# Kernel tuning notes

Hardware: AMD Instinct MI355X
Metric: run time of the kernel (lower is better)

The kernel has to match this reference:

```python
import jax, jax.numpy as jnp
import numpy as np

N, E, H, L = 50000, 1_600_000, 128, 3


def _ln(x, g, b, eps=1e-5):
    m = x.mean(-1, keepdims=True)
    v = x.var(-1, keepdims=True)
    return (x - m) / jnp.sqrt(v + eps) * g + b


def _mlp2(inp, w1, b1, g, be, w2, b2):
    # Linear -> LayerNorm -> SiLU -> (Dropout=identity in eval) -> Linear
    h = inp @ w1 + b1
    h = jax.nn.silu(_ln(h, g, be))
    return h @ w2 + b2


def setup_inputs() -> dict:
    key = jax.random.key(0)
    ks = jax.random.split(key, 16)
    s = 0.05
    inp = {
        'x': jax.random.normal(ks[0], (N, 7), jnp.float32),
        'pos': jax.random.normal(ks[1], (N, 3), jnp.float32),
        'edge_index': jax.random.randint(ks[2], (2, E), 0, N, jnp.int64),
        'enc_w1': jax.random.normal(ks[3], (7, H)) * s,
        'enc_b1': jnp.zeros((H,)),
        'enc_g': jnp.ones((H,)),
        'enc_be': jnp.zeros((H,)),
        'enc_w2': jax.random.normal(ks[4], (H, H)) * s,
        'enc_b2': jnp.zeros((H,)),
        'e_w1': jax.random.normal(ks[5], (L, 2 * H + 5, H)) * s,
        'e_b1': jnp.zeros((L, H)),
        'e_g': jnp.ones((L, H)),
        'e_be': jnp.zeros((L, H)),
        'e_w2': jax.random.normal(ks[6], (L, H, H)) * s,
        'e_b2': jnp.zeros((L, H)),
        'n_w1': jax.random.normal(ks[7], (L, 2 * H, H)) * s,
        'n_b1': jnp.zeros((L, H)),
        'n_g': jnp.ones((L, H)),
        'n_be': jnp.zeros((L, H)),
        'n_w2': jax.random.normal(ks[8], (L, H, H)) * s,
        'n_b2': jnp.zeros((L, H)),
        'ln_g': jnp.ones((L, H)),
        'ln_b': jnp.zeros((L, H)),
        'dec_w1': jax.random.normal(ks[9], (H, H)) * s,
        'dec_b1': jnp.zeros((H,)),
        'dec_w2': jax.random.normal(ks[10], (H, H // 2)) * s,
        'dec_b2': jnp.zeros((H // 2,)),
        'dec_w3': jax.random.normal(ks[11], (H // 2, 6)) * s,
        'dec_b3': jnp.zeros((6,)),
    }
    return inp


def reference(x, pos, edge_index, enc_w1, enc_b1, enc_g, enc_be, enc_w2, enc_b2,
              e_w1, e_b1, e_g, e_be, e_w2, e_b2,
              n_w1, n_b1, n_g, n_be, n_w2, n_b2,
              ln_g, ln_b, dec_w1, dec_b1, dec_w2, dec_b2, dec_w3, dec_b3):
    n_nodes = x.shape[0]
    row, col = edge_index[0], edge_index[1]  # row=source(j), col=target(i)

    # physics edge features: [dist, direction(3), 1/r^2]
    diff = pos[col] - pos[row]                          # (E,3)
    dist = jnp.linalg.norm(diff, axis=-1, keepdims=True) + 1e-8
    edge_attr = jnp.concatenate([dist, diff / dist, 1.0 / (dist ** 2 + 1e-6)], -1)

    h = _mlp2(x, enc_w1, enc_b1, enc_g, enc_be, enc_w2, enc_b2)  # (N,H)

    for l in range(L):
        # message: cat(x_i, x_j, edge_attr) -> edge MLP
        msg_in = jnp.concatenate([h[col], h[row], edge_attr], -1)  # (E,2H+5)
        msg = _mlp2(msg_in, e_w1[l], e_b1[l], e_g[l], e_be[l], e_w2[l], e_b2[l])
        # scatter-add aggregate to targets
        aggr = jax.ops.segment_sum(msg, col, num_segments=n_nodes)  # (N,H)
        # update: cat(x, aggr) -> node MLP, then residual + LayerNorm
        h_new = _mlp2(jnp.concatenate([h, aggr], -1),
                      n_w1[l], n_b1[l], n_g[l], n_be[l], n_w2[l], n_b2[l])
        h = _ln(h + h_new, ln_g[l], ln_b[l])

    d = jax.nn.silu(h @ dec_w1 + dec_b1)
    d = jax.nn.silu(d @ dec_w2 + dec_b2)
    delta = d @ dec_w3 + dec_b3                                  # (N,6)
    return x[:, :6] + delta
```

## Files before the change

kernel.cpp:

```cpp
#include <hip/hip_runtime.h>

typedef unsigned short u16;
typedef unsigned int u32;
typedef __bf16 bf16x8 __attribute__((ext_vector_type(8)));
typedef float f32x4 __attribute__((ext_vector_type(4)));
typedef float f32x2 __attribute__((ext_vector_type(2)));

#define AS_STRIDE 136

__device__ __forceinline__ u16 f2bf1(float f) {
  union { __bf16 h; u16 u; } c; c.h = (__bf16)f; return c.u;
}
__device__ __forceinline__ u32 cvt2bf(float a, float b) {
  union { __bf16 h[2]; u32 u; } c; c.h[0] = (__bf16)a; c.h[1] = (__bf16)b; return c.u;
}
__device__ __forceinline__ float bf2f(u16 u) {
  union { u32 u; float f; } v; v.u = ((u32)u) << 16; return v.f;
}
__device__ __forceinline__ float silu_f(float a) {
  return a * __builtin_amdgcn_rcpf(1.f + __expf(-a));
}
__device__ __forceinline__ float rsq_f(float x) {
  return __builtin_amdgcn_rsqf(x);
}
__device__ __forceinline__ f32x2 unpk2(u32 p) {
  union { u32 u; float f; } a, b;
  a.u = p << 16; b.u = p & 0xffff0000u;
  return (f32x2){a.f, b.f};
}

__global__ void edge_hist(const int* __restrict__ edst, int E, int* __restrict__ cnt) {
  int i = blockIdx.x * blockDim.x + threadIdx.x;
  if (i < E) atomicAdd(&cnt[edst[i]], 1);
}

__global__ __launch_bounds__(1024)
void scan_kernel(const int* __restrict__ cnt, int* __restrict__ cursor, int Nn) {
  __shared__ int part[1024];
  int t = threadIdx.x;
  int per = (Nn + 1023) / 1024;
  int b = t * per;
  int s = 0;
  for (int i = 0; i < per; i++) { int idx = b + i; if (idx < Nn) s += cnt[idx]; }
  part[t] = s;
  __syncthreads();
  for (int d = 1; d < 1024; d <<= 1) {
    int v = (t >= d) ? part[t - d] : 0;
    __syncthreads();
    part[t] += v;
    __syncthreads();
  }
  int excl = (t == 0) ? 0 : part[t - 1];
  for (int i = 0; i < per; i++) {
    int idx = b + i;
    if (idx < Nn) { cursor[idx] = excl; excl += cnt[idx]; }
  }
}

__global__ void edge_scatter(const int* __restrict__ esrc, const int* __restrict__ edst,
                             int E, int* __restrict__ cursor,
                             int* __restrict__ ssrc, int* __restrict__ sdst) {
  int i = blockIdx.x * blockDim.x + threadIdx.x;
  if (i < E) {
    int d = edst[i];
    int p = atomicAdd(&cursor[d], 1);
    ssrc[p] = esrc[i];
    sdst[p] = d;
  }
}

__global__ void prep_weights(const float* __restrict__ e_w1, const float* __restrict__ e_w2,
                             const float* __restrict__ n_w1, const float* __restrict__ n_w2,
                             u16* __restrict__ eW1T, u16* __restrict__ eW2T,
                             u16* __restrict__ nW1T, u16* __restrict__ nW2T) {
  int i = blockIdx.x * blockDim.x + threadIdx.x;
  const int s1 = 3 * 128 * 256;
  const int s2 = 3 * 128 * 128;
  if (i < s1) {
    int l = i / 32768, r = i % 32768, n = r >> 8, k = r & 255;
    eW1T[i] = f2bf1(e_w1[l * 33408 + k * 128 + n]);
  } else if (i < s1 + s2) {
    int j = i - s1; int l = j / 16384, r = j % 16384, n = r >> 7, k = r & 127;
    eW2T[j] = f2bf1(e_w2[l * 16384 + k * 128 + n]);
  } else if (i < s1 + s2 + s1) {
    int j = i - s1 - s2; int l = j / 32768, r = j % 32768, n = r >> 8, k = r & 255;
    nW1T[j] = f2bf1(n_w1[l * 32768 + k * 128 + n]);
  } else if (i < 2 * s1 + 2 * s2) {
    int j = i - 2 * s1 - s2; int l = j / 16384, r = j % 16384, n = r >> 7, k = r & 127;
    nW2T[j] = f2bf1(n_w2[l * 16384 + k * 128 + n]);
  }
}

__global__ void prep_weights2(const float* __restrict__ enc_w1, const float* __restrict__ enc_w2,
                              const float* __restrict__ dec_w1, const float* __restrict__ dec_w2,
                              const float* __restrict__ dec_w3, const float* __restrict__ e_w1,
                              u16* __restrict__ encW1T, u16* __restrict__ encW2T,
                              u16* __restrict__ decW1T, u16* __restrict__ decW2T,
                              u16* __restrict__ decW3T, u16* __restrict__ eW1cT) {
  int i = blockIdx.x * blockDim.x + threadIdx.x;
  if (i < 4096) {
    int n = i >> 5, k = i & 31;
    encW1T[i] = (k < 7) ? f2bf1(enc_w1[k * 128 + n]) : (u16)0;
  } else if (i < 20480) {
    int j = i - 4096; int n = j >> 7, k = j & 127;
    encW2T[j] = f2bf1(enc_w2[k * 128 + n]);
  } else if (i < 36864) {
    int j = i - 20480; int n = j >> 7, k = j & 127;
    decW1T[j] = f2bf1(dec_w1[k * 128 + n]);
  } else if (i < 45056) {
    int j = i - 36864; int n = j >> 7, k = j & 127;
    decW2T[j] = f2bf1(dec_w2[k * 64 + n]);
  } else if (i < 46080) {
    int j = i - 45056; int n = j >> 6, k = j & 63;
    decW3T[j] = (n < 6) ? f2bf1(dec_w3[k * 6 + n]) : (u16)0;
  } else if (i < 58368) {
    int j = i - 46080; int l = j / 4096, r = j % 4096, n = r >> 5, k = r & 31;
    eW1cT[j] = (k < 5) ? f2bf1(e_w1[l * 33408 + (256 + k) * 128 + n]) : (u16)0;
  }
}

__global__ __launch_bounds__(256, 4)
void encoder_mfma(const float* __restrict__ x,
                  const u16* __restrict__ W1T,
                  const float* __restrict__ b1,
                  const float* __restrict__ g, const float* __restrict__ be,
                  const u16* __restrict__ W2T,
                  const float* __restrict__ b2,
                  const u16* __restrict__ eW1T0,
                  const float* __restrict__ eb10,
                  u16* __restrict__ hbf, u16* __restrict__ hd_all,
                  u16* __restrict__ hs_all, int Nn) {
  __shared__ __align__(16) u16 As[64 * 40];
  __shared__ __align__(16) u16 ts[64 * AS_STRIDE];
  const int tid = threadIdx.x;
  const int m0 = blockIdx.x * 64;
  const int w = tid >> 6, lane = tid & 63, quad = lane >> 4, l16 = lane & 15;
  const int c0w = w * 32;

  if (tid < 64) {
    int node = m0 + tid; if (node >= Nn) node = Nn - 1;
    union { u16 us[32]; uint4 v[4]; } pk;
    #pragma unroll
    for (int k = 0; k < 32; k++) pk.us[k] = 0;
    #pragma unroll
    for (int k = 0; k < 7; k++) pk.us[k] = f2bf1(x[node * 7 + k]);
    #pragma unroll
    for (int k = 0; k < 4; k++) *(uint4*)(As + tid * 40 + k * 8) = pk.v[k];
  }
  __syncthreads();

  f32x4 acc[4][2];
  #pragma unroll
  for (int rt = 0; rt < 4; rt++)
    #pragma unroll
    for (int ct = 0; ct < 2; ct++)
      acc[rt][ct] = (f32x4){0.f, 0.f, 0.f, 0.f};
  {
    const int kl = quad * 8;
    bf16x8 af[4];
    #pragma unroll
    for (int rt = 0; rt < 4; rt++)
      af[rt] = *(const bf16x8*)(As + (rt * 16 + l16) * 40 + kl);
    #pragma unroll
    for (int ct = 0; ct < 2; ct++) {
      bf16x8 bfv = *(const bf16x8*)(W1T + (c0w + ct * 16 + l16) * 32 + kl);
      #pragma unroll
      for (int rt = 0; rt < 4; rt++)
        acc[rt][ct] = __builtin_amdgcn_mfma_f32_16x16x32_bf16(af[rt], bfv, acc[rt][ct], 0, 0, 0);
    }
  }
  #pragma unroll
  for (int ct = 0; ct < 2; ct++) {
    int n = c0w + ct * 16 + l16;
    float b1v = b1[n];
    #pragma unroll
    for (int rt = 0; rt < 4; rt++)
      #pragma unroll
      for (int r = 0; r < 4; r++)
        ts[(rt * 16 + quad * 4 + r) * AS_STRIDE + n] = f2bf1(acc[rt][ct][r] + b1v);
  }
  __syncthreads();

  {
    int row = tid >> 2, sub = tid & 3;
    float s = 0.f, sq = 0.f, vals[32];
    #pragma unroll
    for (int i = 0; i < 32; i++) {
      float v = bf2f(ts[row * AS_STRIDE + sub + i * 4]);
      vals[i] = v; s += v; sq += v * v;
    }
    s += __shfl_xor(s, 1); sq += __shfl_xor(sq, 1);
    s += __shfl_xor(s, 2); sq += __shfl_xor(sq, 2);
    float mean = s * (1.f / 128.f);
    float rstd = rsq_f(sq * (1.f / 128.f) - mean * mean + 1e-5f);
    #pragma unroll
    for (int i = 0; i < 32; i++) {
      int c = sub + i * 4;
      float a = (vals[i] - mean) * rstd * g[c] + be[c];
      ts[row * AS_STRIDE + c] = f2bf1(silu_f(a));
    }
  }
  __syncthreads();

  f32x4 acc2[4][2];
  #pragma unroll
  for (int rt = 0; rt < 4; rt++)
    #pragma unroll
    for (int ct = 0; ct < 2; ct++)
      acc2[rt][ct] = (f32x4){0.f, 0.f, 0.f, 0.f};
  #pragma unroll
  for (int kk = 0; kk < 4; kk++) {
    const int kl = kk * 32 + quad * 8;
    bf16x8 af[4];
    #pragma unroll
    for (int rt = 0; rt < 4; rt++)
      af[rt] = *(const bf16x8*)(ts + (rt * 16 + l16) * AS_STRIDE + kl);
    #pragma unroll
    for (int ct = 0; ct < 2; ct++) {
      bf16x8 bfv = *(const bf16x8*)(W2T + (size_t)(c0w + ct * 16 + l16) * 128 + kl);
      #pragma unroll
      for (int rt = 0; rt < 4; rt++)
        acc2[rt][ct] = __builtin_amdgcn_mfma_f32_16x16x32_bf16(af[rt], bfv, acc2[rt][ct], 0, 0, 0);
    }
  }
  __syncthreads();
  #pragma unroll
  for (int ct = 0; ct < 2; ct++) {
    int n = c0w + ct * 16 + l16;
    float b2v = b2[n];
    #pragma unroll
    for (int rt = 0; rt < 4; rt++)
      #pragma unroll
      for (int r = 0; r < 4; r++) {
        int m = rt * 16 + quad * 4 + r;
        int node = m0 + m;
        u16 hb = f2bf1(acc2[rt][ct][r] + b2v);
        ts[m * AS_STRIDE + n] = hb;
        if (node < Nn) hbf[(size_t)node * 128 + n] = hb;
      }
  }
  __syncthreads();

  {
    f32x4 ah[4][2];
    #pragma unroll
    for (int rt = 0; rt < 4; rt++)
      #pragma unroll
      for (int ct = 0; ct < 2; ct++)
        ah[rt][ct] = (f32x4){0.f, 0.f, 0.f, 0.f};
    #pragma unroll
    for (int kk = 0; kk < 4; kk++) {
      const int kl = kk * 32 + quad * 8;
      bf16x8 af[4];
      #pragma unroll
      for (int rt = 0; rt < 4; rt++)
        af[rt] = *(const bf16x8*)(ts + (rt * 16 + l16) * AS_STRIDE + kl);
      #pragma unroll
      for (int ct = 0; ct < 2; ct++) {
        bf16x8 bd = *(const bf16x8*)(eW1T0 + (size_t)(c0w + ct * 16 + l16) * 256 + kl);
        #pragma unroll
        for (int rt = 0; rt < 4; rt++)
          ah[rt][ct] = __builtin_amdgcn_mfma_f32_16x16x32_bf16(af[rt], bd, ah[rt][ct], 0, 0, 0);
      }
    }
    #pragma unroll
    for (int ct = 0; ct < 2; ct++) {
      int n = c0w + ct * 16 + l16;
      float b1v = eb10[n];
      #pragma unroll
      for (int rt = 0; rt < 4; rt++)
        #pragma unroll
        for (int r = 0; r < 4; r++) {
          int node = m0 + rt * 16 + quad * 4 + r;
          if (node < Nn) hd_all[(size_t)node * 128 + n] = f2bf1(ah[rt][ct][r] + b1v);
        }
    }
    #pragma unroll
    for (int rt = 0; rt < 4; rt++)
      #pragma unroll
      for (int ct = 0; ct < 2; ct++)
        ah[rt][ct] = (f32x4){0.f, 0.f, 0.f, 0.f};
    #pragma unroll
    for (int kk = 0; kk < 4; kk++) {
      const int kl = kk * 32 + quad * 8;
      bf16x8 af[4];
      #pragma unroll
      for (int rt = 0; rt < 4; rt++)
        af[rt] = *(const bf16x8*)(ts + (rt * 16 + l16) * AS_STRIDE + kl);
      #pragma unroll
      for (int ct = 0; ct < 2; ct++) {
        bf16x8 bs = *(const bf16x8*)(eW1T0 + (size_t)(c0w + ct * 16 + l16) * 256 + 128 + kl);
        #pragma unroll
        for (int rt = 0; rt < 4; rt++)
          ah[rt][ct] = __builtin_amdgcn_mfma_f32_16x16x32_bf16(af[rt], bs, ah[rt][ct], 0, 0, 0);
      }
    }
    #pragma unroll
    for (int ct = 0; ct < 2; ct++) {
      int n = c0w + ct * 16 + l16;
      #pragma unroll
      for (int rt = 0; rt < 4; rt++)
        #pragma unroll
        for (int r = 0; r < 4; r++) {
          int node = m0 + rt * 16 + quad * 4 + r;
          if (node < Nn) hs_all[(size_t)node * 128 + n] = f2bf1(ah[rt][ct][r]);
        }
    }
  }
}

__global__ __launch_bounds__(256, 4)
void edge_mlp_kernel(const int* __restrict__ ssrc, const int* __restrict__ sdst,
                     const float* __restrict__ pos,
                     const u16* __restrict__ hd_all, const u16* __restrict__ hs_all,
                     const u16* __restrict__ w1cT,
                     const float* __restrict__ g, const float* __restrict__ be,
                     const u16* __restrict__ W2T,
                     const float* __restrict__ b2,
                     float* __restrict__ aggr) {
  __shared__ int s_dst[64];
  __shared__ __align__(16) u16 s_eaA[64 * 40];
  __shared__ __align__(16) u16 s_t[64 * AS_STRIDE];
  __shared__ __align__(16) u16 s_msg[128 * 68];

  const int tid = threadIdx.x;
  const int bid = blockIdx.x;
  const int e0 = ((bid & 7) * (gridDim.x >> 3) + (bid >> 3)) * 64;
  const int w = tid >> 6, lane = tid & 63, quad = lane >> 4, l16 = lane & 15;
  const int c0w = w * 32;
  const int rg = tid >> 4, cg = tid & 15;
  const int c0 = cg * 8;

  int pdst[4], psrc[4];
  #pragma unroll
  for (int rr = 0; rr < 4; rr++) {
    pdst[rr] = sdst[e0 + rg * 4 + rr];
    psrc[rr] = ssrc[e0 + rg * 4 + rr];
  }
  uint4 hd4[4], hs4[4];
  #pragma unroll
  for (int rr = 0; rr < 4; rr++) {
    hd4[rr] = *(const uint4*)(hd_all + (size_t)pdst[rr] * 128 + c0);
    hs4[rr] = *(const uint4*)(hs_all + (size_t)psrc[rr] * 128 + c0);
  }
  asm volatile("" ::: "memory");

  if (tid < 64) {
    int src = ssrc[e0 + tid], dst = sdst[e0 + tid];
    s_dst[tid] = dst;
    float dx = pos[dst * 3 + 0] - pos[src * 3 + 0];
    float dy = pos[dst * 3 + 1] - pos[src * 3 + 1];
    float dz = pos[dst * 3 + 2] - pos[src * 3 + 2];
    float dist = sqrtf(dx * dx + dy * dy + dz * dz) + 1e-8f;
    float inv = __builtin_amdgcn_rcpf(dist);
    union { u16 us[40]; uint4 v[5]; } pk;
    #pragma unroll
    for (int k = 0; k < 40; k++) pk.us[k] = 0;
    pk.us[0] = f2bf1(dist);
    pk.us[1] = f2bf1(dx * inv); pk.us[2] = f2bf1(dy * inv); pk.us[3] = f2bf1(dz * inv);
    pk.us[4] = f2bf1(__builtin_amdgcn_rcpf(dist * dist + 1e-6f));
    #pragma unroll
    for (int k = 0; k < 5; k++) *(uint4*)(s_eaA + tid * 40 + k * 8) = pk.v[k];
  }
  __syncthreads();

  {
    f32x4 ae[4][2];
    #pragma unroll
    for (int rt = 0; rt < 4; rt++)
      #pragma unroll
      for (int ct = 0; ct < 2; ct++)
        ae[rt][ct] = (f32x4){0.f, 0.f, 0.f, 0.f};
    const int kl = quad * 8;
    bf16x8 afe[4];
    #pragma unroll
    for (int rt = 0; rt < 4; rt++)
      afe[rt] = *(const bf16x8*)(s_eaA + (rt * 16 + l16) * 40 + kl);
    #pragma unroll
    for (int ct = 0; ct < 2; ct++) {
      bf16x8 bw = *(const bf16x8*)(w1cT + (c0w + ct * 16 + l16) * 32 + kl);
      #pragma unroll
      for (int rt = 0; rt < 4; rt++)
        ae[rt][ct] = __builtin_amdgcn_mfma_f32_16x16x32_bf16(afe[rt], bw, ae[rt][ct], 0, 0, 0);
    }
    #pragma unroll
    for (int ct = 0; ct < 2; ct++) {
      int n = c0w + ct * 16 + l16;
      #pragma unroll
      for (int rt = 0; rt < 4; rt++)
        #pragma unroll
        for (int r = 0; r < 4; r++)
          s_t[(rt * 16 + quad * 4 + r) * AS_STRIDE + n] = f2bf1(ae[rt][ct][r]);
    }
  }
  __syncthreads();

  {
    f32x2 g2[4], be2[4];
    {
      f32x4 ga = *(const f32x4*)(g + c0), gb = *(const f32x4*)(g + c0 + 4);
      f32x4 ba = *(const f32x4*)(be + c0), bb = *(const f32x4*)(be + c0 + 4);
      g2[0] = (f32x2){ga[0], ga[1]}; g2[1] = (f32x2){ga[2], ga[3]};
      g2[2] = (f32x2){gb[0], gb[1]}; g2[3] = (f32x2){gb[2], gb[3]};
      be2[0] = (f32x2){ba[0], ba[1]}; be2[1] = (f32x2){ba[2], ba[3]};
      be2[2] = (f32x2){bb[0], bb[1]}; be2[3] = (f32x2){bb[2], bb[3]};
    }
    #pragma unroll
    for (int rr = 0; rr < 4; rr++) {
      int m = rg * 4 + rr;
      uint4 te4 = *(const uint4*)(s_t + m * AS_STRIDE + c0);
      u32 hp[4] = {hd4[rr].x, hd4[rr].y, hd4[rr].z, hd4[rr].w};
      u32 sp[4] = {hs4[rr].x, hs4[rr].y, hs4[rr].z, hs4[rr].w};
      u32 tp[4] = {te4.x, te4.y, te4.z, te4.w};
      f32x2 t2[4], sm2 = (f32x2){0.f, 0.f}, sq2 = (f32x2){0.f, 0.f};
      #pragma unroll
      for (int p = 0; p < 4; p++) {
        t2[p] = unpk2(hp[p]) + unpk2(sp[p]) + unpk2(tp[p]);
        sm2 += t2[p];
        sq2 += t2[p] * t2[p];
      }
      float sm = sm2[0] + sm2[1], sq = sq2[0] + sq2[1];
      sm += __shfl_xor(sm, 1);  sq += __shfl_xor(sq, 1);
      sm += __shfl_xor(sm, 2);  sq += __shfl_xor(sq, 2);
      sm += __shfl_xor(sm, 4);  sq += __shfl_xor(sq, 4);
      sm += __shfl_xor(sm, 8);  sq += __shfl_xor(sq, 8);
      float mean = sm * (1.f / 128.f);
      float rstd = rsq_f(sq * (1.f / 128.f) - mean * mean + 1e-5f);
      f32x2 sc = (f32x2){rstd, rstd};
      f32x2 ofs = (f32x2){-mean * rstd, -mean * rstd};
      float o[8];
      #pragma unroll
      for (int p = 0; p < 4; p++) {
        f32x2 a = t2[p] * sc + ofs;
        a = a * g2[p] + be2[p];
        o[2 * p]     = silu_f(a[0]);
        o[2 * p + 1] = silu_f(a[1]);
      }
      uint4 st;
      st.x = cvt2bf(o[0], o[1]); st.y = cvt2bf(o[2], o[3]);
      st.z = cvt2bf(o[4], o[5]); st.w = cvt2bf(o[6], o[7]);
      *(uint4*)(s_t + m * AS_STRIDE + c0) = st;
    }
  }
  __syncthreads();

  f32x4 acc2[4][2];
  #pragma unroll
  for (int rt = 0; rt < 4; rt++)
    #pragma unroll
    for (int ct = 0; ct < 2; ct++)
      acc2[rt][ct] = (f32x4){0.f, 0.f, 0.f, 0.f};

  #pragma unroll
  for (int kk = 0; kk < 4; kk++) {
    const int kl = kk * 32 + quad * 8;
    bf16x8 af[4];
    #pragma unroll
    for (int rt = 0; rt < 4; rt++)
      af[rt] = *(const bf16x8*)(s_t + (rt * 16 + l16) * AS_STRIDE + kl);
    #pragma unroll
    for (int ct = 0; ct < 2; ct++) {
      bf16x8 bfv = *(const bf16x8*)(W2T + (size_t)(c0w + ct * 16 + l16) * 128 + kl);
      #pragma unroll
      for (int rt = 0; rt < 4; rt++)
        acc2[rt][ct] = __builtin_amdgcn_mfma_f32_16x16x32_bf16(af[rt], bfv, acc2[rt][ct], 0, 0, 0);
    }
  }

  #pragma unroll
  for (int ct = 0; ct < 2; ct++) {
    int n = c0w + ct * 16 + l16;
    float b2v = b2[n];
    #pragma unroll
    for (int rt = 0; rt < 4; rt++) {
      int mb = rt * 16 + quad * 4;
      uint2 st;
      st.x = cvt2bf(acc2[rt][ct][0] + b2v, acc2[rt][ct][1] + b2v);
      st.y = cvt2bf(acc2[rt][ct][2] + b2v, acc2[rt][ct][3] + b2v);
      *(uint2*)(s_msg + n * 68 + mb) = st;
    }
  }
  __syncthreads();

  {
    int c = tid & 127, q = tid >> 7;
    int r0 = q * 32;
    const u16* mp = s_msg + c * 68 + r0;
    float run = 0.f; int cur = s_dst[r0];
    #pragma unroll
    for (int i = 0; i < 8; i++) {
      uint2 pr = *(const uint2*)(mp + 4 * i);
      union { u32 u; float f; } va, vb, vc, vd;
      va.u = pr.x << 16; vb.u = pr.x & 0xffff0000u;
      vc.u = pr.y << 16; vd.u = pr.y & 0xffff0000u;
      int rb = r0 + 4 * i;
      int d0 = s_dst[rb], d1 = s_dst[rb + 1], d2 = s_dst[rb + 2], d3 = s_dst[rb + 3];
      if (d0 != cur) { atomicAdd(&aggr[(size_t)cur * 128 + c], run); run = 0.f; cur = d0; }
      run += va.f;
      if (d1 != cur) { atomicAdd(&aggr[(size_t)cur * 128 + c], run); run = 0.f; cur = d1; }
      run += vb.f;
      if (d2 != cur) { atomicAdd(&aggr[(size_t)cur * 128 + c], run); run = 0.f; cur = d2; }
      run += vc.f;
      if (d3 != cur) { atomicAdd(&aggr[(size_t)cur * 128 + c], run); run = 0.f; cur = d3; }
      run += vd.f;
    }
    atomicAdd(&aggr[(size_t)cur * 128 + c], run);
  }
}

__global__ __launch_bounds__(256, 4)
void node_mlp_kernel(u16* __restrict__ hbf, float* __restrict__ aggr,
                     const u16* __restrict__ W1T, const float* __restrict__ b1,
                     const float* __restrict__ g, const float* __restrict__ be,
                     const u16* __restrict__ W2T, const float* __restrict__ b2,
                     const float* __restrict__ lng, const float* __restrict__ lnb,
                     const u16* __restrict__ W1Tn, const float* __restrict__ b1n,
                     u16* __restrict__ hd_all, u16* __restrict__ hs_all,
                     const float* __restrict__ x,
                     const u16* __restrict__ dW1T, const float* __restrict__ db1,
                     const u16* __restrict__ dW2T, const float* __restrict__ db2,
                     const u16* __restrict__ dW3T, const float* __restrict__ db3,
                     float* __restrict__ out,
                     int Nn) {
  __shared__ __align__(16) u16 As[128 * AS_STRIDE];
  u16* t_su = As;
  u16* u_su = As + 64 * AS_STRIDE;

  const int tid = threadIdx.x;
  const int m0 = blockIdx.x * 64;
  const int w = tid >> 6, lane = tid & 63, quad = lane >> 4, l16 = lane & 15;
  const int c0w = w * 32;

  {
    int r = tid >> 4, c8 = (tid & 15) * 8;
    const float4 z4 = {0.f, 0.f, 0.f, 0.f};
    #pragma unroll
    for (int rp = 0; rp < 4; rp++) {
      int m = rp * 16 + r;
      int node = m0 + m; if (node >= Nn) node = Nn - 1;
      *(uint4*)(As + m * AS_STRIDE + c8) = *(const uint4*)(hbf + (size_t)node * 128 + c8);
      float* ap = aggr + (size_t)node * 128 + c8;
      float4 f0 = *(const float4*)ap;
      float4 f1 = *(const float4*)(ap + 4);
      uint4 pk;
      pk.x = cvt2bf(f0.x, f0.y); pk.y = cvt2bf(f0.z, f0.w);
      pk.z = cvt2bf(f1.x, f1.y); pk.w = cvt2bf(f1.z, f1.w);
      *(uint4*)(As + (64 + m) * AS_STRIDE + c8) = pk;
      *(float4*)ap = z4;
      *(float4*)(ap + 4) = z4;
    }
  }
  __syncthreads();

  f32x4 acc[4][2];
  #pragma unroll
  for (int rt = 0; rt < 4; rt++)
    #pragma unroll
    for (int ct = 0; ct < 2; ct++)
      acc[rt][ct] = (f32x4){0.f, 0.f, 0.f, 0.f};

  #pragma unroll
  for (int kk = 0; kk < 8; kk++) {
    const u16* Ab = As + (kk < 4 ? 0 : 64 * AS_STRIDE);
    const int kl = (kk & 3) * 32 + quad * 8;
    bf16x8 af[4];
    #pragma unroll
    for (int rt = 0; rt < 4; rt++)
      af[rt] = *(const bf16x8*)(Ab + (rt * 16 + l16) * AS_STRIDE + kl);
    const int kg = kk * 32 + quad * 8;
    #pragma unroll
    for (int ct = 0; ct < 2; ct++) {
      bf16x8 bfv = *(const bf16x8*)(W1T + (size_t)(c0w + ct * 16 + l16) * 256 + kg);
      #pragma unroll
      for (int rt = 0; rt < 4; rt++)
        acc[rt][ct] = __builtin_amdgcn_mfma_f32_16x16x32_bf16(af[rt], bfv, acc[rt][ct], 0, 0, 0);
    }
  }

  float b1v[2];
  #pragma unroll
  for (int ct = 0; ct < 2; ct++) b1v[ct] = b1[c0w + ct * 16 + l16];
  __syncthreads();

  #pragma unroll
  for (int rt = 0; rt < 4; rt++)
    #pragma unroll
    for (int ct = 0; ct < 2; ct++) {
      int n = c0w + ct * 16 + l16;
      #pragma unroll
      for (int r = 0; r < 4; r++)
        t_su[(rt * 16 + quad * 4 + r) * AS_STRIDE + n] = f2bf1(acc[rt][ct][r] + b1v[ct]);
    }
  __syncthreads();

  {
    int row = tid >> 2, sub = tid & 3;
    float s = 0.f, sq = 0.f, vals[32];
    #pragma unroll
    for (int i = 0; i < 32; i++) {
      float v = bf2f(t_su[row * AS_STRIDE + sub + i * 4]);
      vals[i] = v; s += v; sq += v * v;
    }
    s += __shfl_xor(s, 1); sq += __shfl_xor(sq, 1);
    s += __shfl_xor(s, 2); sq += __shfl_xor(sq, 2);
    float mean = s * (1.f / 128.f);
    float rstd = rsq_f(sq * (1.f / 128.f) - mean * mean + 1e-5f);
    #pragma unroll
    for (int i = 0; i < 32; i++) {
      int c = sub + i * 4;
      float a = (vals[i] - mean) * rstd * g[c] + be[c];
      u_su[row * AS_STRIDE + c] = f2bf1(silu_f(a));
    }
  }
  __syncthreads();

  f32x4 acc2[4][2];
  #pragma unroll
  for (int rt = 0; rt < 4; rt++)
    #pragma unroll
    for (int ct = 0; ct < 2; ct++)
      acc2[rt][ct] = (f32x4){0.f, 0.f, 0.f, 0.f};

  #pragma unroll
  for (int kk = 0; kk < 4; kk++) {
    const int kl = kk * 32 + quad * 8;
    bf16x8 af[4];
    #pragma unroll
    for (int rt = 0; rt < 4; rt++)
      af[rt] = *(const bf16x8*)(u_su + (rt * 16 + l16) * AS_STRIDE + kl);
    #pragma unroll
    for (int ct = 0; ct < 2; ct++) {
      bf16x8 bfv = *(const bf16x8*)(W2T + (size_t)(c0w + ct * 16 + l16) * 128 + kl);
      #pragma unroll
      for (int rt = 0; rt < 4; rt++)
        acc2[rt][ct] = __builtin_amdgcn_mfma_f32_16x16x32_bf16(af[rt], bfv, acc2[rt][ct], 0, 0, 0);
    }
  }
  __syncthreads();

  #pragma unroll
  for (int ct = 0; ct < 2; ct++) {
    int n = c0w + ct * 16 + l16;
    float b2v = b2[n];
    #pragma unroll
    for (int rt = 0; rt < 4; rt++)
      #pragma unroll
      for (int r = 0; r < 4; r++) {
        int m = rt * 16 + quad * 4 + r;
        int node = m0 + m; if (node >= Nn) node = Nn - 1;
        t_su[m * AS_STRIDE + n] =
            f2bf1(acc2[rt][ct][r] + b2v + bf2f(hbf[(size_t)node * 128 + n]));
      }
  }
  __syncthreads();

  {
    int row = tid >> 2, sub = tid & 3;
    int node = m0 + row;
    float s = 0.f, sq = 0.f, vals[32];
    #pragma unroll
    for (int i = 0; i < 32; i++) {
      float v = bf2f(t_su[row * AS_STRIDE + sub + i * 4]);
      vals[i] = v; s += v; sq += v * v;
    }
    s += __shfl_xor(s, 1); sq += __shfl_xor(sq, 1);
    s += __shfl_xor(s, 2); sq += __shfl_xor(sq, 2);
    float mean = s * (1.f / 128.f);
    float rstd = rsq_f(sq * (1.f / 128.f) - mean * mean + 1e-5f);
    #pragma unroll
    for (int i = 0; i < 32; i++) {
      int c = sub + i * 4;
      float v = (vals[i] - mean) * rstd * lng[c] + lnb[c];
      u16 hb = f2bf1(v);
      t_su[row * AS_STRIDE + c] = hb;
      if (node < Nn) hbf[(size_t)node * 128 + c] = hb;
    }
  }

  if (W1Tn != nullptr) {
    __syncthreads();
    f32x4 ah[4][2];
    #pragma unroll
    for (int rt = 0; rt < 4; rt++)
      #pragma unroll
      for (int ct = 0; ct < 2; ct++)
        ah[rt][ct] = (f32x4){0.f, 0.f, 0.f, 0.f};
    #pragma unroll
    for (int kk = 0; kk < 4; kk++) {
      const int kl = kk * 32 + quad * 8;
      bf16x8 af[4];
      #pragma unroll
      for (int rt = 0; rt < 4; rt++)
        af[rt] = *(const bf16x8*)(t_su + (rt * 16 + l16) * AS_STRIDE + kl);
      #pragma unroll
      for (int ct = 0; ct < 2; ct++) {
        bf16x8 bd = *(const bf16x8*)(W1Tn + (size_t)(c0w + ct * 16 + l16) * 256 + kl);
        #pragma unroll
        for (int rt = 0; rt < 4; rt++)
          ah[rt][ct] = __builtin_amdgcn_mfma_f32_16x16x32_bf16(af[rt], bd, ah[rt][ct], 0, 0, 0);
      }
    }
    #pragma unroll
    for (int ct = 0; ct < 2; ct++) {
      int n = c0w + ct * 16 + l16;
      float bv = b1n[n];
      #pragma unroll
      for (int rt = 0; rt < 4; rt++)
        #pragma unroll
        for (int r = 0; r < 4; r++) {
          int node = m0 + rt * 16 + quad * 4 + r;
          if (node < Nn) hd_all[(size_t)node * 128 + n] = f2bf1(ah[rt][ct][r] + bv);
        }
    }
    #pragma unroll
    for (int rt = 0; rt < 4; rt++)
      #pragma unroll
      for (int ct = 0; ct < 2; ct++)
        ah[rt][ct] = (f32x4){0.f, 0.f, 0.f, 0.f};
    #pragma unroll
    for (int kk = 0; kk < 4; kk++) {
      const int kl = kk * 32 + quad * 8;
      bf16x8 af[4];
      #pragma unroll
      for (int rt = 0; rt < 4; rt++)
        af[rt] = *(const bf16x8*)(t_su + (rt * 16 + l16) * AS_STRIDE + kl);
      #pragma unroll
      for (int ct = 0; ct < 2; ct++) {
        bf16x8 bs = *(const bf16x8*)(W1Tn + (size_t)(c0w + ct * 16 + l16) * 256 + 128 + kl);
        #pragma unroll
        for (int rt = 0; rt < 4; rt++)
          ah[rt][ct] = __builtin_amdgcn_mfma_f32_16x16x32_bf16(af[rt], bs, ah[rt][ct], 0, 0, 0);
      }
    }
    #pragma unroll
    for (int ct = 0; ct < 2; ct++) {
      int n = c0w + ct * 16 + l16;
      #pragma unroll
      for (int rt = 0; rt < 4; rt++)
        #pragma unroll
        for (int r = 0; r < 4; r++) {
          int node = m0 + rt * 16 + quad * 4 + r;
          if (node < Nn) hs_all[(size_t)node * 128 + n] = f2bf1(ah[rt][ct][r]);
        }
    }
  }

  if (dW1T != nullptr) {
    __syncthreads();
    f32x4 da[4][2];
    #pragma unroll
    for (int rt = 0; rt < 4; rt++)
      #pragma unroll
      for (int ct = 0; ct < 2; ct++)
        da[rt][ct] = (f32x4){0.f, 0.f, 0.f, 0.f};
    #pragma unroll
    for (int kk = 0; kk < 4; kk++) {
      const int kl = kk * 32 + quad * 8;
      bf16x8 af[4];
      #pragma unroll
      for (int rt = 0; rt < 4; rt++)
        af[rt] = *(const bf16x8*)(t_su + (rt * 16 + l16) * AS_STRIDE + kl);
      #pragma unroll
      for (int ct = 0; ct < 2; ct++) {
        bf16x8 bfv = *(const bf16x8*)(dW1T + (size_t)(c0w + ct * 16 + l16) * 128 + kl);
        #pragma unroll
        for (int rt = 0; rt < 4; rt++)
          da[rt][ct] = __builtin_amdgcn_mfma_f32_16x16x32_bf16(af[rt], bfv, da[rt][ct], 0, 0, 0);
      }
    }
    __syncthreads();
    #pragma unroll
    for (int ct = 0; ct < 2; ct++) {
      int n = c0w + ct * 16 + l16;
      float bv = db1[n];
      #pragma unroll
      for (int rt = 0; rt < 4; rt++)
        #pragma unroll
        for (int r = 0; r < 4; r++)
          u_su[(rt * 16 + quad * 4 + r) * AS_STRIDE + n] = f2bf1(silu_f(da[rt][ct][r] + bv));
    }
    __syncthreads();
    {
      const int c0b = w * 16;
      f32x4 a2[4];
      #pragma unroll
      for (int rt = 0; rt < 4; rt++) a2[rt] = (f32x4){0.f, 0.f, 0.f, 0.f};
      #pragma unroll
      for (int kk = 0; kk < 4; kk++) {
        const int kl = kk * 32 + quad * 8;
        bf16x8 af[4];
        #pragma unroll
        for (int rt = 0; rt < 4; rt++)
          af[rt] = *(const bf16x8*)(u_su + (rt * 16 + l16) * AS_STRIDE + kl);
        bf16x8 bfv = *(const bf16x8*)(dW2T + (size_t)(c0b + l16) * 128 + kl);
        #pragma unroll
        for (int rt = 0; rt < 4; rt++)
          a2[rt] = __builtin_amdgcn_mfma_f32_16x16x32_bf16(af[rt], bfv, a2[rt], 0, 0, 0);
      }
      float bv = db2[c0b + l16];
      #pragma unroll
      for (int rt = 0; rt < 4; rt++)
        #pragma unroll
        for (int r = 0; r < 4; r++)
          t_su[(rt * 16 + quad * 4 + r) * 72 + c0b + l16] = f2bf1(silu_f(a2[rt][r] + bv));
    }
    __syncthreads();
    if (w == 0) {
      f32x4 a3[4];
      #pragma unroll
      for (int rt = 0; rt < 4; rt++) a3[rt] = (f32x4){0.f, 0.f, 0.f, 0.f};
      #pragma unroll
      for (int kk = 0; kk < 2; kk++) {
        const int kl = kk * 32 + quad * 8;
        bf16x8 af[4];
        #pragma unroll
        for (int rt = 0; rt < 4; rt++)
          af[rt] = *(const bf16x8*)(t_su + (rt * 16 + l16) * 72 + kl);
        bf16x8 bfv = *(const bf16x8*)(dW3T + l16 * 64 + kl);
        #pragma unroll
        for (int rt = 0; rt < 4; rt++)
          a3[rt] = __builtin_amdgcn_mfma_f32_16x16x32_bf16(af[rt], bfv, a3[rt], 0, 0, 0);
      }
      if (l16 < 6) {
        float bv = db3[l16];
        #pragma unroll
        for (int rt = 0; rt < 4; rt++)
          #pragma unroll
          for (int r = 0; r < 4; r++) {
            int node = m0 + rt * 16 + quad * 4 + r;
            if (node < Nn)
              out[(size_t)node * 6 + l16] = a3[rt][r] + bv + x[node * 7 + l16];
          }
      }
    }
  }
}

extern "C" void kernel_launch(void* const* d_in, const int* in_sizes, int n_in,
                              void* d_out, int out_size, void* d_ws, size_t ws_size,
                              hipStream_t stream) {
  const float* x      = (const float*)d_in[0];
  const float* pos    = (const float*)d_in[1];
  const int*   eidx   = (const int*)d_in[2];
  const float* enc_w1 = (const float*)d_in[3];
  const float* enc_b1 = (const float*)d_in[4];
  const float* enc_g  = (const float*)d_in[5];
  const float* enc_be = (const float*)d_in[6];
  const float* enc_w2 = (const float*)d_in[7];
  const float* enc_b2 = (const float*)d_in[8];
  const float* e_w1   = (const float*)d_in[9];
  const float* e_b1   = (const float*)d_in[10];
  const float* e_g    = (const float*)d_in[11];
  const float* e_be   = (const float*)d_in[12];
  const float* e_w2   = (const float*)d_in[13];
  const float* e_b2   = (const float*)d_in[14];
  const float* n_w1   = (const float*)d_in[15];
  const float* n_b1   = (const float*)d_in[16];
  const float* n_g    = (const float*)d_in[17];
  const float* n_be   = (const float*)d_in[18];
  const float* n_w2   = (const float*)d_in[19];
  const float* n_b2   = (const float*)d_in[20];
  const float* ln_g   = (const float*)d_in[21];
  const float* ln_b   = (const float*)d_in[22];
  const float* dec_w1 = (const float*)d_in[23];
  const float* dec_b1 = (const float*)d_in[24];
  const float* dec_w2 = (const float*)d_in[25];
  const float* dec_b2 = (const float*)d_in[26];
  const float* dec_w3 = (const float*)d_in[27];
  const float* dec_b3 = (const float*)d_in[28];

  const int N = in_sizes[0] / 7;
  const int E = in_sizes[2] / 2;

  char* ws = (char*)d_ws;
  size_t off = 0;
  u16*   hbf    = (u16*)(ws + off);   off += (size_t)N * 128 * 2;
  u16*   hd_all = (u16*)(ws + off);   off += (size_t)N * 128 * 2;
  u16*   hs_all = (u16*)(ws + off);   off += (size_t)N * 128 * 2;
  float* aggr   = (float*)(ws + off); off += (size_t)N * 128 * 4;
  u16* eW1T = (u16*)(ws + off); off += 3 * 128 * 256 * 2;
  u16* eW2T = (u16*)(ws + off); off += 3 * 128 * 128 * 2;
  u16* nW1T = (u16*)(ws + off); off += 3 * 128 * 256 * 2;
  u16* nW2T = (u16*)(ws + off); off += 3 * 128 * 128 * 2;
  u16* encW1T = (u16*)(ws + off); off += 128 * 32 * 2;
  u16* encW2T = (u16*)(ws + off); off += 128 * 128 * 2;
  u16* decW1T = (u16*)(ws + off); off += 128 * 128 * 2;
  u16* decW2T = (u16*)(ws + off); off += 64 * 128 * 2;
  u16* decW3T = (u16*)(ws + off); off += 16 * 64 * 2;
  u16* eW1cT  = (u16*)(ws + off); off += 3 * 128 * 32 * 2;
  int* cnt    = (int*)(ws + off); off += (size_t)N * 4;
  int* cursor = (int*)(ws + off); off += (size_t)N * 4;
  int* ssrc   = (int*)(ws + off); off += (size_t)E * 4;
  int* sdst   = (int*)(ws + off); off += (size_t)E * 4;

  hipMemsetAsync(cnt, 0, (size_t)N * 4, stream);
  edge_hist<<<(E + 255) / 256, 256, 0, stream>>>(eidx + E, E, cnt);
  scan_kernel<<<1, 1024, 0, stream>>>(cnt, cursor, N);
  edge_scatter<<<(E + 255) / 256, 256, 0, stream>>>(eidx, eidx + E, E, cursor, ssrc, sdst);

  prep_weights<<<1152, 256, 0, stream>>>(e_w1, e_w2, n_w1, n_w2, eW1T, eW2T, nW1T, nW2T);
  prep_weights2<<<228, 256, 0, stream>>>(enc_w1, enc_w2, dec_w1, dec_w2, dec_w3, e_w1,
                                         encW1T, encW2T, decW1T, decW2T, decW3T, eW1cT);

  hipMemsetAsync(aggr, 0, (size_t)N * 128 * 4, stream);

  const int nblk = (N + 63) / 64;
  encoder_mfma<<<nblk, 256, 0, stream>>>(x, encW1T, enc_b1, enc_g, enc_be, encW2T, enc_b2,
                                         eW1T, e_b1, hbf, hd_all, hs_all, N);

  for (int l = 0; l < 3; l++) {
    edge_mlp_kernel<<<E / 64, 256, 0, stream>>>(
        ssrc, sdst, pos, hd_all, hs_all,
        eW1cT + (size_t)l * 4096,
        e_g + l * 128, e_be + l * 128,
        eW2T + (size_t)l * 128 * 128, e_b2 + l * 128, aggr);
    const u16* W1Tn = (l < 2) ? (eW1T + (size_t)(l + 1) * 128 * 256) : (const u16*)nullptr;
    const bool last = (l == 2);
    node_mlp_kernel<<<nblk, 256, 0, stream>>>(
        hbf, aggr,
        nW1T + (size_t)l * 128 * 256, n_b1 + l * 128, n_g + l * 128, n_be + l * 128,
        nW2T + (size_t)l * 128 * 128, n_b2 + l * 128,
        ln_g + l * 128, ln_b + l * 128,
        W1Tn, e_b1 + ((l + 1) % 3) * 128, hd_all, hs_all,
        x,
        last ? decW1T : (const u16*)nullptr, dec_b1,
        last ? decW2T : (const u16*)nullptr, dec_b2,
        last ? decW3T : (const u16*)nullptr, dec_b3,
        (float*)d_out, N);
  }
}
```

Before: 1.226 ms.

## Scatter edge messages directly from MFMA accumulators, dropping shared-memory staging

The edge kernel now run-length reduces each lane's 16 output rows straight from the MFMA accumulator registers and issues atomics for them, instead of first writing bf16 messages to a shared buffer, syncing, and re-reading them. This removes a shared-memory round trip, a barrier and the bf16 rounding of messages, and the smaller LDS footprint allows raising the occupancy hint from 4 to 6 blocks. In exchange each lane's runs cover only 16 rows rather than 32, so more atomics may be issued, and the higher occupancy target may force register spills.

```diff
diff --git a/kernel.cpp b/kernel.cpp
--- a/kernel.cpp
+++ b/kernel.cpp
@@ -309,7 +309,7 @@
   }
 }
 
-__global__ __launch_bounds__(256, 4)
+__global__ __launch_bounds__(256, 6)
 void edge_mlp_kernel(const int* __restrict__ ssrc, const int* __restrict__ sdst,
                      const float* __restrict__ pos,
                      const u16* __restrict__ hd_all, const u16* __restrict__ hs_all,
@@ -321,7 +321,6 @@
   __shared__ int s_dst[64];
   __shared__ __align__(16) u16 s_eaA[64 * 40];
   __shared__ __align__(16) u16 s_t[64 * AS_STRIDE];
-  __shared__ __align__(16) u16 s_msg[128 * 68];
 
   const int tid = threadIdx.x;
   const int bid = blockIdx.x;
@@ -467,44 +466,32 @@
     }
   }
 
-  #pragma unroll
-  for (int ct = 0; ct < 2; ct++) {
-    int n = c0w + ct * 16 + l16;
-    float b2v = b2[n];
-    #pragma unroll
-    for (int rt = 0; rt < 4; rt++) {
-      int mb = rt * 16 + quad * 4;
-      uint2 st;
-      st.x = cvt2bf(acc2[rt][ct][0] + b2v, acc2[rt][ct][1] + b2v);
-      st.y = cvt2bf(acc2[rt][ct][2] + b2v, acc2[rt][ct][3] + b2v);
-      *(uint2*)(s_msg + n * 68 + mb) = st;
-    }
-  }
-  __syncthreads();
-
   {
-    int c = tid & 127, q = tid >> 7;
-    int r0 = q * 32;
-    const u16* mp = s_msg + c * 68 + r0;
-    float run = 0.f; int cur = s_dst[r0];
-    #pragma unroll
-    for (int i = 0; i < 8; i++) {
-      uint2 pr = *(const uint2*)(mp + 4 * i);
-      union { u32 u; float f; } va, vb, vc, vd;
-      va.u = pr.x << 16; vb.u = pr.x & 0xffff0000u;
-      vc.u = pr.y << 16; vd.u = pr.y & 0xffff0000u;
-      int rb = r0 + 4 * i;
-      int d0 = s_dst[rb], d1 = s_dst[rb + 1], d2 = s_dst[rb + 2], d3 = s_dst[rb + 3];
-      if (d0 != cur) { atomicAdd(&aggr[(size_t)cur * 128 + c], run); run = 0.f; cur = d0; }
-      run += va.f;
-      if (d1 != cur) { atomicAdd(&aggr[(size_t)cur * 128 + c], run); run = 0.f; cur = d1; }
-      run += vb.f;
-      if (d2 != cur) { atomicAdd(&aggr[(size_t)cur * 128 + c], run); run = 0.f; cur = d2; }
-      run += vc.f;
-      if (d3 != cur) { atomicAdd(&aggr[(size_t)cur * 128 + c], run); run = 0.f; cur = d3; }
-      run += vd.f;
-    }
-    atomicAdd(&aggr[(size_t)cur * 128 + c], run);
+    int dv[16];
+    #pragma unroll
+    for (int rt = 0; rt < 4; rt++)
+      #pragma unroll
+      for (int r = 0; r < 4; r++)
+        dv[rt * 4 + r] = s_dst[rt * 16 + quad * 4 + r];
+
+    #pragma unroll
+    for (int ct = 0; ct < 2; ct++) {
+      const int n = c0w + ct * 16 + l16;
+      const float b2v = b2[n];
+      float* ap = aggr + n;
+      int cur = dv[0];
+      float run = 0.f;
+      #pragma unroll
+      for (int i = 0; i < 16; i++) {
+        int d = dv[i];
+        if (d != cur) {
+          atomicAdd(ap + (size_t)cur * 128, run);
+          run = 0.f; cur = d;
+        }
+        run += acc2[i >> 2][ct][i & 3] + b2v;
+      }
+      atomicAdd(ap + (size_t)cur * 128, run);
+    }
   }
 }
 
```

Measured after the change: 1.515 ms. 23.6% more time.
